# Kernel optimization log

Hardware: AMD Instinct MI355X
Metric: run time of the kernel (lower is better)

The kernel has to match this reference:

```python
import jax, jax.numpy as jnp
import numpy as np

H = 256  # hidden_dim
N = 500000  # num_orbitals
M = 8192  # num_molecules


def setup_inputs() -> dict:
    key = jax.random.key(0)
    ks = jax.random.split(key, 12)
    s = lambda fan_in: 1.0 / np.sqrt(fan_in)
    inp = {
        "orbital_embeddings": jax.random.normal(ks[0], (N, H), dtype=jnp.float32),
        "batch": jnp.sort(jax.random.randint(ks[1], (N,), 0, M, dtype=jnp.int32)),
        "num_molecules": M,
        # attention MLP: Linear(H, H//2) -> ReLU -> Linear(H//2, 1)
        "aW1": jax.random.uniform(ks[2], (H, H // 2), jnp.float32, -s(H), s(H)),
        "ab1": jnp.zeros((H // 2,), jnp.float32),
        "aW2": jax.random.uniform(ks[3], (H // 2, 1), jnp.float32, -s(H // 2), s(H // 2)),
        "ab2": jnp.zeros((1,), jnp.float32),
        # global head: Linear(H,H)->ReLU->Linear(H,H//2)->ReLU->Linear(H//2,1)
        "gW1": jax.random.uniform(ks[4], (H, H), jnp.float32, -s(H), s(H)),
        "gb1": jnp.zeros((H,), jnp.float32),
        "gW2": jax.random.uniform(ks[5], (H, H // 2), jnp.float32, -s(H), s(H)),
        "gb2": jnp.zeros((H // 2,), jnp.float32),
        "gW3": jax.random.uniform(ks[6], (H // 2, 1), jnp.float32, -s(H // 2), s(H // 2)),
        "gb3": jnp.zeros((1,), jnp.float32),
    }
    return inp


def reference(orbital_embeddings, batch, num_molecules, aW1, ab1, aW2, ab2,
              gW1, gb1, gW2, gb2, gW3, gb3):
    # attention logits: [N, 1] (dropout is identity in eval mode)
    h = jax.nn.relu(orbital_embeddings @ aW1 + ab1)
    logits = h @ aW2 + ab2  # [N, 1]

    # per-molecule (segment) softmax over orbitals, numerically stable
    lg = logits[:, 0]  # [N]
    seg_max = jax.ops.segment_max(lg, batch, num_segments=num_molecules)  # [M]
    seg_max = jnp.where(jnp.isfinite(seg_max), seg_max, 0.0)  # empty segments
    ex = jnp.exp(lg - seg_max[batch])  # [N]
    denom = jax.ops.segment_sum(ex, batch, num_segments=num_molecules)  # [M]
    w = ex / denom[batch]  # [N]

    # weighted scatter-add pooling -> [M, H]
    weighted = orbital_embeddings * w[:, None]
    mol = jax.ops.segment_sum(weighted, batch, num_segments=num_molecules)

    # global head MLP -> [M, 1]
    g = jax.nn.relu(mol @ gW1 + gb1)
    g = jax.nn.relu(g @ gW2 + gb2)
    return g @ gW3 + gb3
```

## Files before the change

### kernel.cpp

```cpp
#include <hip/hip_runtime.h>
#include <hip/hip_bf16.h>

#define H      256
#define CAP    32
#define GRID12 512
#define RPW    8

typedef _Float16 f16x8 __attribute__((ext_vector_type(8)));
typedef float    f32x4 __attribute__((ext_vector_type(4)));

#define AS3(p) ((__attribute__((address_space(3))) void*)(p))
#define AS1(p) ((const __attribute__((address_space(1))) void*)(p))

#define VMWAIT8() asm volatile("s_waitcnt vmcnt(8)" ::: "memory")
#define VMWAIT0() asm volatile("s_waitcnt vmcnt(0)" ::: "memory")
#define LGKM0()   asm volatile("s_waitcnt lgkmcnt(0)" ::: "memory")
#define SBAR()    __builtin_amdgcn_s_barrier()
#define SCHED0()  __builtin_amdgcn_sched_barrier(0)

__global__ __launch_bounds__(256) void k0_pack(
    const float* __restrict__ aW1, const float* __restrict__ gW1,
    const float* __restrict__ gW2,
    _Float16* __restrict__ aW1F, float* __restrict__ gW1P, float* __restrict__ gW2P)
{
    int idx = blockIdx.x * 256 + threadIdx.x;
    int stride = gridDim.x * 256;
    for (int e8 = idx; e8 < 4096; e8 += stride) {
        int l = e8 & 63, kknt = e8 >> 6;
        int kk = kknt & 7, nt = kknt >> 3;
        int j = nt*16 + (l & 15);
        int kbase = kk*32 + (l >> 4)*8;
        f16x8 v;
        #pragma unroll
        for (int e = 0; e < 8; ++e) v[e] = (_Float16)aW1[(kbase + e)*128 + j];
        *reinterpret_cast<f16x8*>(aW1F + e8*8) = v;
    }
    for (int e = idx; e < 64*256*4; e += stride) {
        int s = e & 3, j = (e >> 2) & 255, kq = e >> 10;
        gW1P[e] = gW1[(kq*4+s)*256 + j];
    }
    for (int e = idx; e < 64*128*4; e += stride) {
        int s = e & 3, j = (e >> 2) & 127, kq = e >> 9;
        gW2P[e] = gW2[(kq*4+s)*128 + j];
    }
}

__global__ __launch_bounds__(256) void k2a_starts(
    const int* __restrict__ batch, int* __restrict__ starts, int N, int M)
{
    int i = blockIdx.x * 256 + threadIdx.x;
    if (i >= N) return;
    int b = batch[i];
    if (i == 0) {
        for (int m = 0; m <= b; ++m) starts[m] = 0;
    } else {
        int p = batch[i-1];
        for (int m = p + 1; m <= b; ++m) starts[m] = i;
    }
    if (i == N - 1) {
        for (int m = b + 1; m <= M; ++m) starts[m] = N;
    }
}

__global__ __launch_bounds__(256) void k12_fused(
    const float* __restrict__ emb, const int* __restrict__ starts,
    const _Float16* __restrict__ aW1F, const float* __restrict__ ab1,
    const float* __restrict__ aW2, const float* __restrict__ ab2,
    float* __restrict__ mol, int M)
{
    __shared__ __align__(16) float ef[2][CAP * H];
    __shared__ float pr[4][CAP];
    __shared__ float wl[CAP];

    const int t = threadIdx.x, w = t >> 6, l = t & 63;
    const f32x4 zero = {0.f, 0.f, 0.f, 0.f};

    f16x8 bf[2][8];
    #pragma unroll
    for (int nt2 = 0; nt2 < 2; ++nt2)
        #pragma unroll
        for (int kk = 0; kk < 8; ++kk)
            bf[nt2][kk] = *reinterpret_cast<const f16x8*>(
                aW1F + (size_t)(((2*w + nt2)*8 + kk)*64 + l)*8);

    float b1v[2], w2v[2];
    #pragma unroll
    for (int nt2 = 0; nt2 < 2; ++nt2) {
        int j = 32*w + nt2*16 + (l & 15);
        b1v[nt2] = ab1[j];
        w2v[nt2] = aW2[j];
    }
    const float bo = ab2[0];

    int m = blockIdx.x, start = 0, end = 0;
    for (;;) {
        if (m >= M) return;
        start = starts[m]; end = starts[m + 1];
        if (start < end) break;
        mol[(size_t)m*H + t] = 0.f;
        m += GRID12;
    }

    int c0 = start;
    int cc = min(CAP, end - c0);

#define ISSUE8(BUF, C0, CC) do {                                                 \
    char* dst_ = reinterpret_cast<char*>(ef[BUF]);                               \
    _Pragma("unroll")                                                            \
    for (int i_ = 0; i_ < RPW; ++i_) {                                           \
        int r_  = w*RPW + i_;                                                    \
        int rr_ = r_ < (CC) ? r_ : (CC) - 1;                                     \
        const char* gs_ = reinterpret_cast<const char*>(                         \
            emb + (size_t)((C0) + rr_)*H) + ((l*16) ^ ((rr_ & 7) << 4));         \
        __builtin_amdgcn_global_load_lds(AS1(gs_), AS3(dst_ + r_*1024), 16, 0, 0);\
    } } while (0)

    ISSUE8(0, c0, cc);
    int cur = 0;
    float mx = -INFINITY, s = 0.f, acc = 0.f;

    for (;;) {
        const int  cur_m = m, cur_cc = cc;
        const bool last_chunk = (c0 + CAP >= end);

        int nm = m, nc0 = c0 + CAP, nend = end;
        bool have_next = true;
        if (last_chunk) {
            nm = m + GRID12;
            for (;;) {
                if (nm >= M) { have_next = false; break; }
                int ns = starts[nm], ne = starts[nm + 1];
                if (ns < ne) { nc0 = ns; nend = ne; break; }
                mol[(size_t)nm*H + t] = 0.f;
                nm += GRID12;
            }
        }
        int ncc = have_next ? min(CAP, nend - nc0) : 0;

        SBAR();

        if (have_next) {
            ISSUE8(cur ^ 1, nc0, ncc);
            VMWAIT8();
        } else {
            VMWAIT0();
        }
        SCHED0();
        SBAR();

        const char* bufb = reinterpret_cast<const char*>(ef[cur]);

        const int nr = (cur_cc + 15) >> 4;
        for (int rt = 0; rt < nr; ++rt) {
            int row   = rt*16 + (l & 15);
            int rbase = row*1024 + (l >> 4)*32;
            int swz   = (row & 7) << 4;
            f32x4 a20 = zero, a21 = zero;
            #pragma unroll
            for (int kk = 0; kk < 8; ++kk) {
                int rb = rbase + kk*128;
                float4 a0 = *reinterpret_cast<const float4*>(bufb + ( rb       ^ swz));
                float4 a1 = *reinterpret_cast<const float4*>(bufb + ((rb + 16) ^ swz));
                f16x8 af;
                af[0]=(_Float16)a0.x; af[1]=(_Float16)a0.y; af[2]=(_Float16)a0.z; af[3]=(_Float16)a0.w;
                af[4]=(_Float16)a1.x; af[5]=(_Float16)a1.y; af[6]=(_Float16)a1.z; af[7]=(_Float16)a1.w;
                a20 = __builtin_amdgcn_mfma_f32_16x16x32_f16(af, bf[0][kk], a20, 0, 0, 0);
                a21 = __builtin_amdgcn_mfma_f32_16x16x32_f16(af, bf[1][kk], a21, 0, 0, 0);
            }
            #pragma unroll
            for (int r = 0; r < 4; ++r) {
                float h0 = a20[r] + b1v[0]; h0 = h0 > 0.f ? h0 : 0.f;
                float h1 = a21[r] + b1v[1]; h1 = h1 > 0.f ? h1 : 0.f;
                float p = h0*w2v[0] + h1*w2v[1];
                p += __shfl_xor(p, 1, 64);
                p += __shfl_xor(p, 2, 64);
                p += __shfl_xor(p, 4, 64);
                p += __shfl_xor(p, 8, 64);
                if ((l & 15) == 0) pr[w][rt*16 + (l >> 4)*4 + r] = p;
            }
        }
        LGKM0(); SCHED0();
        SBAR();

        float lg = -INFINITY;
        if (l < cur_cc) lg = pr[0][l] + pr[1][l] + pr[2][l] + pr[3][l] + bo;
        float mc = lg;
        mc = fmaxf(mc, __shfl_xor(mc, 1, 64));
        mc = fmaxf(mc, __shfl_xor(mc, 2, 64));
        mc = fmaxf(mc, __shfl_xor(mc, 4, 64));
        mc = fmaxf(mc, __shfl_xor(mc, 8, 64));
        mc = fmaxf(mc, __shfl_xor(mc, 16, 64));
        mc = fmaxf(mc, __shfl_xor(mc, 32, 64));
        float mxn = fmaxf(mx, mc);
        float rsc = __expf(mx - mxn);
        float e = (l < cur_cc) ? __expf(lg - mxn) : 0.f;
        float sc = e;
        sc += __shfl_xor(sc, 1, 64);
        sc += __shfl_xor(sc, 2, 64);
        sc += __shfl_xor(sc, 4, 64);
        sc += __shfl_xor(sc, 8, 64);
        sc += __shfl_xor(sc, 16, 64);
        sc += __shfl_xor(sc, 32, 64);
        s = s*rsc + sc;
        mx = mxn;
        if (w == 0 && l < CAP) wl[l] = e;
        LGKM0(); SCHED0();
        SBAR();

        acc *= rsc;
        #pragma unroll 8
        for (int g = 0; g < cur_cc; ++g) {
            float ev = *reinterpret_cast<const float*>(
                bufb + ((g*1024 + t*4) ^ ((g & 7) << 4)));
            acc += wl[g] * ev;
        }

        if (last_chunk) {
            mol[(size_t)cur_m*H + t] = acc / s;
            mx = -INFINITY; s = 0.f; acc = 0.f;
        }
        if (!have_next) return;
        m = nm; c0 = nc0; end = nend; cc = ncc;
        cur ^= 1;
    }
#undef ISSUE8
}

__global__ __launch_bounds__(256) void k3_mlp(
    const float* __restrict__ mol, const float* __restrict__ gW1P,
    const float* __restrict__ gb1, const float* __restrict__ gW2P,
    const float* __restrict__ gb2, const float* __restrict__ gW3,
    const float* __restrict__ gb3, float* __restrict__ out, int M)
{
    __shared__ __align__(16) float mt[32 * 256];
    __shared__ __align__(16) float g1[32 * 256];
    __shared__ float tmp[4][16];
    int t = threadIdx.x;
    int blk = blockIdx.x;

    #pragma unroll
    for (int i = 0; i < 8; ++i) {
        int f = t + i*256;
        long gidx = (long)blk*2048 + f;
        float4 v = make_float4(0.f,0.f,0.f,0.f);
        if (gidx < (long)M*64) v = reinterpret_cast<const float4*>(mol)[gidx];
        reinterpret_cast<float4*>(mt)[f] = v;
    }
    __syncthreads();

    int j = t & 127, mh = t >> 7;

    float a0[16], a1[16];
    #pragma unroll
    for (int m = 0; m < 16; ++m) { a0[m] = 0.f; a1[m] = 0.f; }
    for (int kq = 0; kq < 64; ++kq) {
        float4 w0 = reinterpret_cast<const float4*>(gW1P)[kq*256 + j];
        float4 w1 = reinterpret_cast<const float4*>(gW1P)[kq*256 + j + 128];
        #pragma unroll
        for (int m = 0; m < 16; ++m) {
            float4 e = *reinterpret_cast<const float4*>(&mt[(mh*16 + m)*256 + kq*4]);
            a0[m] += e.x*w0.x + e.y*w0.y + e.z*w0.z + e.w*w0.w;
            a1[m] += e.x*w1.x + e.y*w1.y + e.z*w1.z + e.w*w1.w;
        }
    }
    {
        float b0 = gb1[j], b1 = gb1[j + 128];
        #pragma unroll
        for (int m = 0; m < 16; ++m) {
            float v0 = a0[m] + b0; v0 = v0 > 0.f ? v0 : 0.f;
            float v1 = a1[m] + b1; v1 = v1 > 0.f ? v1 : 0.f;
            g1[(mh*16 + m)*256 + j]       = v0;
            g1[(mh*16 + m)*256 + j + 128] = v1;
        }
    }
    __syncthreads();

    float a2[16];
    #pragma unroll
    for (int m = 0; m < 16; ++m) a2[m] = 0.f;
    for (int kq = 0; kq < 64; ++kq) {
        float4 w = reinterpret_cast<const float4*>(gW2P)[kq*128 + j];
        #pragma unroll
        for (int m = 0; m < 16; ++m) {
            float4 e = *reinterpret_cast<const float4*>(&g1[(mh*16 + m)*256 + kq*4]);
            a2[m] += e.x*w.x + e.y*w.y + e.z*w.z + e.w*w.w;
        }
    }

    float b2 = gb2[j], w3 = gW3[j];
    float p[16];
    #pragma unroll
    for (int m = 0; m < 16; ++m) {
        float v = a2[m] + b2; v = v > 0.f ? v : 0.f;
        p[m] = v * w3;
    }
    #pragma unroll
    for (int off = 32; off >= 1; off >>= 1) {
        #pragma unroll
        for (int m = 0; m < 16; ++m) p[m] += __shfl_xor(p[m], off, 64);
    }
    int wid = t >> 6;
    if ((t & 63) == 0) {
        #pragma unroll
        for (int m = 0; m < 16; ++m) tmp[wid][m] = p[m];
    }
    __syncthreads();
    if (t < 32) {
        int om = blk*32 + t;
        if (om < M) out[om] = tmp[(t >> 4)*2][t & 15] + tmp[(t >> 4)*2 + 1][t & 15] + gb3[0];
    }
}

extern "C" void kernel_launch(void* const* d_in, const int* in_sizes, int n_in,
                              void* d_out, int out_size, void* d_ws, size_t ws_size,
                              hipStream_t stream) {
    const float* emb  = (const float*)d_in[0];
    const int*   batch= (const int*)d_in[1];
    const float* aW1  = (const float*)d_in[3];
    const float* ab1  = (const float*)d_in[4];
    const float* aW2  = (const float*)d_in[5];
    const float* ab2  = (const float*)d_in[6];
    const float* gW1  = (const float*)d_in[7];
    const float* gb1  = (const float*)d_in[8];
    const float* gW2  = (const float*)d_in[9];
    const float* gb2  = (const float*)d_in[10];
    const float* gW3  = (const float*)d_in[11];
    const float* gb3  = (const float*)d_in[12];
    float* outp = (float*)d_out;

    int N = in_sizes[0] / H;
    int M = out_size;

    char* ws = (char*)d_ws;
    size_t off = 0;
    float*     mol    = (float*)(ws + off);    off += (8u<<20);
    _Float16*  aW1F   = (_Float16*)(ws + off); off += 65536;
    float*     gW1P   = (float*)(ws + off);    off += 262144;
    float*     gW2P   = (float*)(ws + off);    off += 131072;
    int*       starts = (int*)(ws + off);      off += (size_t)(M+1)*4;

    int g12 = M < GRID12 ? M : GRID12;

    k0_pack<<<64, 256, 0, stream>>>(aW1, gW1, gW2, aW1F, gW1P, gW2P);
    k2a_starts<<<(N + 255)/256, 256, 0, stream>>>(batch, starts, N, M);
    k12_fused<<<g12, 256, 0, stream>>>(emb, starts, aW1F, ab1, aW2, ab2, mol, M);
    k3_mlp<<<(M + 31)/32, 256, 0, stream>>>(mol, gW1P, gb1, gW2P, gb2, gW3, gb3, outp, M);
}
```

Measured before the change: 276.2 us.

## Double chunk size to 64 rows with 512-thread blocks splitting MFMA rows and columns

The fused attention-pooling kernel now stages 64 orbital rows per chunk instead of 32 and runs 8 waves per block instead of 4, on a grid of 256 blocks. Each wave computes one 16-row tile against half of the hidden columns, so the previous per-wave loop over row tiles goes away. The pooling loop is fully unrolled over the fixed chunk size, relying on zero softmax weights for padded rows. The aim is to handle a typical molecule in one chunk, cutting barrier rounds and per-chunk overhead. In exchange, padded rows in small molecules are always computed, and the block uses 128KB of LDS, which limits it to one block per CU.

```diff
diff --git a/kernel.cpp b/kernel.cpp
--- a/kernel.cpp
+++ b/kernel.cpp
@@ -2,8 +2,9 @@
 #include <hip/hip_bf16.h>
 
 #define H      256
-#define CAP    32
-#define GRID12 512
+#define CAP    64
+#define NT12   512
+#define GRID12 256
 #define RPW    8
 
 typedef _Float16 f16x8 __attribute__((ext_vector_type(8)));
@@ -62,33 +63,34 @@
     }
 }
 
-__global__ __launch_bounds__(256) void k12_fused(
+__global__ __launch_bounds__(NT12, 2) void k12_fused(
     const float* __restrict__ emb, const int* __restrict__ starts,
     const _Float16* __restrict__ aW1F, const float* __restrict__ ab1,
     const float* __restrict__ aW2, const float* __restrict__ ab2,
     float* __restrict__ mol, int M)
 {
     __shared__ __align__(16) float ef[2][CAP * H];
-    __shared__ float pr[4][CAP];
+    __shared__ float prs[2][CAP];
     __shared__ float wl[CAP];
 
     const int t = threadIdx.x, w = t >> 6, l = t & 63;
+    const int wsel = w >> 2, rt = w & 3;
     const f32x4 zero = {0.f, 0.f, 0.f, 0.f};
 
-    f16x8 bf[2][8];
-    #pragma unroll
-    for (int nt2 = 0; nt2 < 2; ++nt2)
+    f16x8 bf[4][8];
+    #pragma unroll
+    for (int nc = 0; nc < 4; ++nc)
         #pragma unroll
         for (int kk = 0; kk < 8; ++kk)
-            bf[nt2][kk] = *reinterpret_cast<const f16x8*>(
-                aW1F + (size_t)(((2*w + nt2)*8 + kk)*64 + l)*8);
-
-    float b1v[2], w2v[2];
-    #pragma unroll
-    for (int nt2 = 0; nt2 < 2; ++nt2) {
-        int j = 32*w + nt2*16 + (l & 15);
-        b1v[nt2] = ab1[j];
-        w2v[nt2] = aW2[j];
+            bf[nc][kk] = *reinterpret_cast<const f16x8*>(
+                aW1F + (size_t)((((wsel*4 + nc)*8 + kk)*64 + l)*8));
+
+    float b1v[4], w2v[4];
+    #pragma unroll
+    for (int nc = 0; nc < 4; ++nc) {
+        int j = (wsel*4 + nc)*16 + (l & 15);
+        b1v[nc] = ab1[j];
+        w2v[nc] = aW2[j];
     }
     const float bo = ab2[0];
 
@@ -97,7 +99,7 @@
         if (m >= M) return;
         start = starts[m]; end = starts[m + 1];
         if (start < end) break;
-        mol[(size_t)m*H + t] = 0.f;
+        if (t < H) mol[(size_t)m*H + t] = 0.f;
         m += GRID12;
     }
 
@@ -131,13 +133,14 @@
                 if (nm >= M) { have_next = false; break; }
                 int ns = starts[nm], ne = starts[nm + 1];
                 if (ns < ne) { nc0 = ns; nend = ne; break; }
-                mol[(size_t)nm*H + t] = 0.f;
+                if (t < H) mol[(size_t)nm*H + t] = 0.f;
                 nm += GRID12;
             }
         }
         int ncc = have_next ? min(CAP, nend - nc0) : 0;
 
         SBAR();
+        SCHED0();
 
         if (have_next) {
             ISSUE8(cur ^ 1, nc0, ncc);
@@ -147,43 +150,47 @@
         }
         SCHED0();
         SBAR();
+        SCHED0();
 
         const char* bufb = reinterpret_cast<const char*>(ef[cur]);
 
-        const int nr = (cur_cc + 15) >> 4;
-        for (int rt = 0; rt < nr; ++rt) {
-            int row   = rt*16 + (l & 15);
-            int rbase = row*1024 + (l >> 4)*32;
-            int swz   = (row & 7) << 4;
-            f32x4 a20 = zero, a21 = zero;
+        {
+            int row0  = rt*16 + (l & 15);
+            int rbase = row0*1024 + (l >> 4)*32;
+            int swz   = (row0 & 7) << 4;
+            f32x4 c0r = zero, c1r = zero, c2r = zero, c3r = zero;
             #pragma unroll
             for (int kk = 0; kk < 8; ++kk) {
                 int rb = rbase + kk*128;
-                float4 a0 = *reinterpret_cast<const float4*>(bufb + ( rb       ^ swz));
-                float4 a1 = *reinterpret_cast<const float4*>(bufb + ((rb + 16) ^ swz));
+                float4 x0 = *reinterpret_cast<const float4*>(bufb + ( rb       ^ swz));
+                float4 x1 = *reinterpret_cast<const float4*>(bufb + ((rb + 16) ^ swz));
                 f16x8 af;
-                af[0]=(_Float16)a0.x; af[1]=(_Float16)a0.y; af[2]=(_Float16)a0.z; af[3]=(_Float16)a0.w;
-                af[4]=(_Float16)a1.x; af[5]=(_Float16)a1.y; af[6]=(_Float16)a1.z; af[7]=(_Float16)a1.w;
-                a20 = __builtin_amdgcn_mfma_f32_16x16x32_f16(af, bf[0][kk], a20, 0, 0, 0);
-                a21 = __builtin_amdgcn_mfma_f32_16x16x32_f16(af, bf[1][kk], a21, 0, 0, 0);
+                af[0]=(_Float16)x0.x; af[1]=(_Float16)x0.y; af[2]=(_Float16)x0.z; af[3]=(_Float16)x0.w;
+                af[4]=(_Float16)x1.x; af[5]=(_Float16)x1.y; af[6]=(_Float16)x1.z; af[7]=(_Float16)x1.w;
+                c0r = __builtin_amdgcn_mfma_f32_16x16x32_f16(af, bf[0][kk], c0r, 0, 0, 0);
+                c1r = __builtin_amdgcn_mfma_f32_16x16x32_f16(af, bf[1][kk], c1r, 0, 0, 0);
+                c2r = __builtin_amdgcn_mfma_f32_16x16x32_f16(af, bf[2][kk], c2r, 0, 0, 0);
+                c3r = __builtin_amdgcn_mfma_f32_16x16x32_f16(af, bf[3][kk], c3r, 0, 0, 0);
             }
             #pragma unroll
             for (int r = 0; r < 4; ++r) {
-                float h0 = a20[r] + b1v[0]; h0 = h0 > 0.f ? h0 : 0.f;
-                float h1 = a21[r] + b1v[1]; h1 = h1 > 0.f ? h1 : 0.f;
-                float p = h0*w2v[0] + h1*w2v[1];
-                p += __shfl_xor(p, 1, 64);
-                p += __shfl_xor(p, 2, 64);
-                p += __shfl_xor(p, 4, 64);
-                p += __shfl_xor(p, 8, 64);
-                if ((l & 15) == 0) pr[w][rt*16 + (l >> 4)*4 + r] = p;
+                float h, hs = 0.f;
+                h = c0r[r] + b1v[0]; h = h > 0.f ? h : 0.f; hs += h*w2v[0];
+                h = c1r[r] + b1v[1]; h = h > 0.f ? h : 0.f; hs += h*w2v[1];
+                h = c2r[r] + b1v[2]; h = h > 0.f ? h : 0.f; hs += h*w2v[2];
+                h = c3r[r] + b1v[3]; h = h > 0.f ? h : 0.f; hs += h*w2v[3];
+                hs += __shfl_xor(hs, 1, 64);
+                hs += __shfl_xor(hs, 2, 64);
+                hs += __shfl_xor(hs, 4, 64);
+                hs += __shfl_xor(hs, 8, 64);
+                if ((l & 15) == 0) prs[wsel][rt*16 + (l >> 4)*4 + r] = hs;
             }
         }
         LGKM0(); SCHED0();
         SBAR();
-
-        float lg = -INFINITY;
-        if (l < cur_cc) lg = pr[0][l] + pr[1][l] + pr[2][l] + pr[3][l] + bo;
+        SCHED0();
+
+        float lg = (l < cur_cc) ? (prs[0][l] + prs[1][l] + bo) : -INFINITY;
         float mc = lg;
         mc = fmaxf(mc, __shfl_xor(mc, 1, 64));
         mc = fmaxf(mc, __shfl_xor(mc, 2, 64));
@@ -203,20 +210,23 @@
         sc += __shfl_xor(sc, 32, 64);
         s = s*rsc + sc;
         mx = mxn;
-        if (w == 0 && l < CAP) wl[l] = e;
+        if (t < CAP) wl[t] = e;
         LGKM0(); SCHED0();
         SBAR();
+        SCHED0();
 
         acc *= rsc;
-        #pragma unroll 8
-        for (int g = 0; g < cur_cc; ++g) {
-            float ev = *reinterpret_cast<const float*>(
-                bufb + ((g*1024 + t*4) ^ ((g & 7) << 4)));
-            acc += wl[g] * ev;
+        if (t < H) {
+            #pragma unroll
+            for (int g = 0; g < CAP; ++g) {
+                float ev = *reinterpret_cast<const float*>(
+                    bufb + ((g*1024 + t*4) ^ ((g & 7) << 4)));
+                acc += wl[g] * ev;
+            }
         }
 
         if (last_chunk) {
-            mol[(size_t)cur_m*H + t] = acc / s;
+            if (t < H) mol[(size_t)cur_m*H + t] = acc / s;
             mx = -INFINITY; s = 0.f; acc = 0.f;
         }
         if (!have_next) return;
@@ -343,6 +353,6 @@
 
     k0_pack<<<64, 256, 0, stream>>>(aW1, gW1, gW2, aW1F, gW1P, gW2P);
     k2a_starts<<<(N + 255)/256, 256, 0, stream>>>(batch, starts, N, M);
-    k12_fused<<<g12, 256, 0, stream>>>(emb, starts, aW1F, ab1, aW2, ab2, mol, M);
+    k12_fused<<<g12, NT12, 0, stream>>>(emb, starts, aW1F, ab1, aW2, ab2, mol, M);
     k3_mlp<<<(M + 31)/32, 256, 0, stream>>>(mol, gW1P, gb1, gW2P, gb2, gW3, gb3, outp, M);
 }
```

Result: slower. 284.3 us (+2.9%).
